# Kernel optimization log

Measured on AMD Instinct MI355X. Metric: run time of the kernel, lower is better.

## Reference

```python
import jax, jax.numpy as jnp
import numpy as np
from jax import lax

# Static config (matches init_kwargs)
D_MODEL = 1024
EXPAND = 2
D_INNER = D_MODEL * EXPAND          # 2048
HEAD_DIM = 64
N_HEADS = D_INNER // HEAD_DIM       # 32
N_GROUPS = 1
D_STATE = 128
D_CONV = 4
CONV_DIM = D_INNER + 2 * N_GROUPS * D_STATE        # 2304
D_IN_PROJ = 2 * D_INNER + 2 * N_GROUPS * D_STATE + N_HEADS  # 4384
SEQLEN = 8192
LN_EPS = 1e-5


def setup_inputs() -> dict:
    key = jax.random.key(0)
    ks = jax.random.split(key, 6)
    x = jax.random.normal(ks[0], (SEQLEN, D_MODEL), jnp.float32)
    W_in = jax.random.normal(ks[1], (D_IN_PROJ, D_MODEL), jnp.float32) / np.sqrt(D_MODEL)
    W_conv = jax.random.normal(ks[2], (CONV_DIM, 1, D_CONV), jnp.float32) / np.sqrt(D_CONV)
    b_conv = jnp.zeros((CONV_DIM,), jnp.float32)
    # dt_bias init per Mamba2: dt ~ LogUniform(dt_min, dt_max), inverse-softplus
    dt = jnp.exp(jax.random.uniform(ks[3], (N_HEADS,)) * (np.log(0.1) - np.log(0.001)) + np.log(0.001))
    dt = jnp.clip(dt, 1e-4)
    dt_bias = dt + jnp.log(-jnp.expm1(-dt))
    A_log = jnp.log(jax.random.uniform(ks[4], (N_HEADS,), minval=1.0, maxval=16.0))
    D_param = jnp.ones((N_HEADS,), jnp.float32)
    ln_w = jnp.ones((D_INNER,), jnp.float32)
    ln_b = jnp.zeros((D_INNER,), jnp.float32)
    W_out = jax.random.normal(ks[5], (D_MODEL, D_INNER), jnp.float32) / np.sqrt(D_INNER)
    return dict(x=x, W_in=W_in, W_conv=W_conv, b_conv=b_conv, dt_bias=dt_bias,
                A_log=A_log, D_param=D_param, ln_w=ln_w, ln_b=ln_b, W_out=W_out)


def reference(x, W_in, W_conv, b_conv, dt_bias, A_log, D_param, ln_w, ln_b, W_out):
    L = x.shape[0]
    zxbcdt = x @ W_in.T                                   # (L, d_in_proj)
    z = zxbcdt[:, :D_INNER]                               # gate
    xbc = zxbcdt[:, D_INNER:D_INNER + CONV_DIM]           # (L, conv_dim)
    dt = jax.nn.softplus(zxbcdt[:, D_INNER + CONV_DIM:] + dt_bias)  # (L, h)
    # depthwise causal-window conv with SAME padding over the sequence
    lhs = xbc.T[None]                                      # (1, conv_dim, L)
    conv = lax.conv_general_dilated(lhs, W_conv, (1,), 'SAME',
                                    feature_group_count=CONV_DIM,
                                    dimension_numbers=('NCH', 'OIH', 'NCH'))[0]
    xbc = jax.nn.silu((conv + b_conv[:, None]).T)          # (L, conv_dim)
    x_ssm = xbc[:, :D_INNER].reshape(L, N_HEADS, HEAD_DIM)
    B = xbc[:, D_INNER:D_INNER + N_GROUPS * D_STATE].reshape(L, N_GROUPS, D_STATE)
    C = xbc[:, D_INNER + N_GROUPS * D_STATE:].reshape(L, N_GROUPS, D_STATE)
    hpg = N_HEADS // N_GROUPS
    Bh = jnp.repeat(B, hpg, axis=1)                        # (L, h, n)
    Ch = jnp.repeat(C, hpg, axis=1)                        # (L, h, n)
    A = -jnp.exp(A_log)                                    # (h,), negative
    a = jnp.exp(dt * A)                                    # (L, h) per-token decay in (0,1)
    V = x_ssm * dt[..., None]                              # discretized input (L, h, p)
    # non-causal SSD (VSSD): global state H then readout, plus D skip
    H = jnp.einsum('lhn,lh,lhp->hnp', Bh, a, V)            # (h, n, p)
    y = jnp.einsum('lhn,hnp->lhp', Ch, H) + D_param[None, :, None] * x_ssm
    y = y.reshape(L, D_INNER)
    # LayerNorm (eqx default: weight+bias, eps=1e-5), then gate by z
    mu = jnp.mean(y, axis=-1, keepdims=True)
    var = jnp.var(y, axis=-1, keepdims=True)
    y = ((y - mu) / jnp.sqrt(var + LN_EPS)) * ln_w + ln_b
    y = y * z
    return y @ W_out.T                                     # (L, d_model)
```

## Files before the change

kernel.cpp:

```cpp
#include <hip/hip_runtime.h>
#include <hip/hip_bf16.h>
#include <math.h>

#define L_SEQ 8192
#define DM 1024
#define DI 2048
#define NH 32
#define HD 64
#define DS 128
#define CDIM 2304
#define DPROJ 4384
#define NPAD_IN 4608
#define KSPLIT 8
#define OPROWS 2176

typedef short bf16x8 __attribute__((ext_vector_type(8)));
typedef float floatx4 __attribute__((ext_vector_type(4)));
typedef unsigned short u16x4 __attribute__((ext_vector_type(4)));
typedef unsigned short u16x8 __attribute__((ext_vector_type(8)));

#define AS1(p) ((const __attribute__((address_space(1))) void*)(p))
#define AS3(p) ((__attribute__((address_space(3))) void*)(p))

__device__ __forceinline__ float bf2f(unsigned short u) {
  union { unsigned int i; float f; } c; c.i = ((unsigned int)u) << 16; return c.f;
}
__device__ __forceinline__ unsigned short f2bf(float f) {
  return __bfloat16_as_ushort(__float2bfloat16(f));
}

__global__ __launch_bounds__(512, 2)
void gemm256_8ph(const unsigned short* __restrict__ A, int lda,
                 const unsigned short* __restrict__ B, int ldb,
                 unsigned short* __restrict__ C, int ldc,
                 int K, int Nstore) {
  __shared__ __align__(16) char lds[131072];
  const int t = threadIdx.x;
  const int lane = t & 63;
  const int w = t >> 6;
  const int wm = w & 1, wn = w >> 1;
  const int fr = lane & 15, quad = lane >> 4;

  int gx = gridDim.x, gy = gridDim.y;
  int linear = blockIdx.y * gx + blockIdx.x;
  int xcd = linear & 7, loc = linear >> 3;
  int mper = gy >> 3;
  int mt = xcd * mper + loc % mper;
  int nt = loc / mper;
  const int m0 = mt << 8, n0 = nt << 8;
  const int NT = K >> 6;

  floatx4 acc[8][4];
#pragma unroll
  for (int i = 0; i < 8; ++i)
#pragma unroll
    for (int j = 0; j < 4; ++j) acc[i][j] = (floatx4){0.f, 0.f, 0.f, 0.f};
  bf16x8 af[4][2], b0[2][2], b1[2][2];

  auto stA = [&](int buf, int kt, int g) {
#pragma unroll
    for (int i = 0; i < 2; ++i) {
      int o = (i * 512 + t) * 16;
      int os = o ^ (((o >> 7) & 7) << 4);
      int rloc = os >> 7, kb = os & 127;
      int R = ((rloc >> 6) << 7) | (g << 6) | (rloc & 63);
      const unsigned short* src = A + (size_t)(m0 + R) * lda + (kt << 6) + (kb >> 1);
      __builtin_amdgcn_global_load_lds(AS1(src),
          AS3(lds + buf * 32768 + g * 16384 + o), 16, 0, 0);
    }
  };
  auto stB = [&](int buf, int kt, int g) {
#pragma unroll
    for (int i = 0; i < 2; ++i) {
      int o = (i * 512 + t) * 16;
      int os = o ^ (((o >> 7) & 7) << 4);
      int rloc = os >> 7, kb = os & 127;
      int R = ((rloc >> 5) << 6) | (g << 5) | (rloc & 31);
      const unsigned short* src = B + (size_t)(n0 + R) * ldb + (kt << 6) + (kb >> 1);
      __builtin_amdgcn_global_load_lds(AS1(src),
          AS3(lds + 65536 + buf * 32768 + g * 16384 + o), 16, 0, 0);
    }
  };
  auto rdA = [&](int buf, int mi, int ks) -> bf16x8 {
    int rloc = (wm << 6) | ((mi & 3) << 4) | fr;
    return *(const bf16x8*)(lds + buf * 32768 + (mi >> 2) * 16384 + rloc * 128 +
                            (((ks << 6) | (quad << 4)) ^ ((fr & 7) << 4)));
  };
  auto rdB = [&](int buf, int ni, int ks) -> bf16x8 {
    int rloc = (wn << 5) | ((ni & 1) << 4) | fr;
    return *(const bf16x8*)(lds + 65536 + buf * 32768 + (ni >> 1) * 16384 + rloc * 128 +
                            (((ks << 6) | (quad << 4)) ^ ((fr & 7) << 4)));
  };

  stA(0, 0, 0); stB(0, 0, 0); stB(0, 0, 1); stA(0, 0, 1);
  if (NT > 1) { stA(1, 1, 0); stB(1, 1, 0); stB(1, 1, 1); }
  if (NT > 1) asm volatile("s_waitcnt vmcnt(6)" ::: "memory");
  else        asm volatile("s_waitcnt vmcnt(0)" ::: "memory");
  __builtin_amdgcn_s_barrier();

  for (int kt = 0; kt < NT; ++kt) {
    const int buf = kt & 1;
    const bool pf1 = (kt + 1 < NT);
    const bool pf2 = (kt + 2 < NT);
#pragma unroll
    for (int mi = 0; mi < 4; ++mi) { af[mi][0] = rdA(buf, mi, 0); af[mi][1] = rdA(buf, mi, 1); }
#pragma unroll
    for (int ni = 0; ni < 2; ++ni) { b0[ni][0] = rdB(buf, ni, 0); b0[ni][1] = rdB(buf, ni, 1); }
    if (pf1) stA(buf ^ 1, kt + 1, 1);
    asm volatile("s_waitcnt lgkmcnt(8)" ::: "memory");
    __builtin_amdgcn_s_barrier();
    asm volatile("s_waitcnt lgkmcnt(0)" ::: "memory");
    __builtin_amdgcn_s_setprio(1);
#pragma unroll
    for (int mi = 0; mi < 4; ++mi)
#pragma unroll
      for (int ni = 0; ni < 2; ++ni)
#pragma unroll
        for (int ks = 0; ks < 2; ++ks)
          acc[mi][ni] = __builtin_amdgcn_mfma_f32_16x16x32_bf16(af[mi][ks], b0[ni][ks], acc[mi][ni], 0, 0, 0);
    __builtin_amdgcn_s_setprio(0);
    __builtin_amdgcn_s_barrier();
#pragma unroll
    for (int ni = 0; ni < 2; ++ni) { b1[ni][0] = rdB(buf, ni + 2, 0); b1[ni][1] = rdB(buf, ni + 2, 1); }
    if (pf2) stA(buf, kt + 2, 0);
    __builtin_amdgcn_s_barrier();
    asm volatile("s_waitcnt lgkmcnt(0)" ::: "memory");
    __builtin_amdgcn_s_setprio(1);
#pragma unroll
    for (int mi = 0; mi < 4; ++mi)
#pragma unroll
      for (int ni = 0; ni < 2; ++ni)
#pragma unroll
        for (int ks = 0; ks < 2; ++ks)
          acc[mi][ni + 2] = __builtin_amdgcn_mfma_f32_16x16x32_bf16(af[mi][ks], b1[ni][ks], acc[mi][ni + 2], 0, 0, 0);
    __builtin_amdgcn_s_setprio(0);
    __builtin_amdgcn_s_barrier();
#pragma unroll
    for (int mi = 0; mi < 4; ++mi) { af[mi][0] = rdA(buf, mi + 4, 0); af[mi][1] = rdA(buf, mi + 4, 1); }
    if (pf2) stB(buf, kt + 2, 0);
    __builtin_amdgcn_s_barrier();
    asm volatile("s_waitcnt lgkmcnt(0)" ::: "memory");
    __builtin_amdgcn_s_setprio(1);
#pragma unroll
    for (int mi = 0; mi < 4; ++mi)
#pragma unroll
      for (int ni = 0; ni < 2; ++ni)
#pragma unroll
        for (int ks = 0; ks < 2; ++ks)
          acc[mi + 4][ni + 2] = __builtin_amdgcn_mfma_f32_16x16x32_bf16(af[mi][ks], b1[ni][ks], acc[mi + 4][ni + 2], 0, 0, 0);
    __builtin_amdgcn_s_setprio(0);
    __builtin_amdgcn_s_barrier();
    if (pf2) stB(buf, kt + 2, 1);
    __builtin_amdgcn_s_barrier();
    __builtin_amdgcn_s_setprio(1);
#pragma unroll
    for (int mi = 0; mi < 4; ++mi)
#pragma unroll
      for (int ni = 0; ni < 2; ++ni)
#pragma unroll
        for (int ks = 0; ks < 2; ++ks)
          acc[mi + 4][ni] = __builtin_amdgcn_mfma_f32_16x16x32_bf16(af[mi][ks], b0[ni][ks], acc[mi + 4][ni], 0, 0, 0);
    __builtin_amdgcn_s_setprio(0);
    if (kt < NT - 1) {
      if (pf2) asm volatile("s_waitcnt vmcnt(6)" ::: "memory");
      else     asm volatile("s_waitcnt vmcnt(0)" ::: "memory");
      __builtin_amdgcn_s_barrier();
    }
  }

  unsigned short* rp = (unsigned short*)lds;
  const int mb = wm * 128, nb = wn * 64;
#pragma unroll
  for (int mi = 0; mi < 8; ++mi)
#pragma unroll
    for (int ni = 0; ni < 4; ++ni)
#pragma unroll
      for (int r = 0; r < 4; ++r)
        rp[(mb + mi * 16 + quad * 4 + r) * 256 + nb + ni * 16 + fr] = f2bf(acc[mi][ni][r]);
  __syncthreads();
#pragma unroll
  for (int j = 0; j < 16; ++j) {
    int lin = j * 4096 + t * 8;
    int row = lin >> 8, col = lin & 255;
    int gcol = n0 + col;
    if (gcol < Nstore)
      *(u16x8*)&C[(size_t)(m0 + row) * ldc + gcol] = *(const u16x8*)&rp[lin];
  }
}

template <int MODE>
__global__ __launch_bounds__(256)
void gemm_bt_mfma(const unsigned short* __restrict__ A, int lda,
                  const unsigned short* __restrict__ B, int ldb,
                  void* __restrict__ Cout, int ldc,
                  int Kfull, int Nstore,
                  const unsigned short* __restrict__ xs,
                  const float* __restrict__ Dvec) {
  __shared__ __align__(16) char smem[17408];
  unsigned short* Asm = (unsigned short*)smem;
  unsigned short* Bsm = Asm + 128 * 32;
  const int t = threadIdx.x;

  int bx = blockIdx.x, by = blockIdx.y;
  if (MODE != 2) {
    int gx = gridDim.x;
    int linear = by * gx + bx;
    int xcd = linear & 7;
    int local = linear >> 3;
    by = xcd * 8 + (local & 7);
    bx = local >> 3;
  }
  const int m0 = by * 128;
  const int n0 = bx * 128;

  int kstart = 0, klen = Kfull;
  if (MODE == 2) { klen = Kfull / KSPLIT; kstart = blockIdx.z * klen; }
  const int wave = t >> 6, lane = t & 63;
  const int wm = (wave & 1) * 64;
  const int wn = (wave >> 1) * 64;
  const int fr = lane & 15;
  const int quad = lane >> 4;

  floatx4 acc[4][4];
#pragma unroll
  for (int i = 0; i < 4; ++i)
#pragma unroll
    for (int j = 0; j < 4; ++j) acc[i][j] = (floatx4){0.f, 0.f, 0.f, 0.f};

  for (int k0 = kstart; k0 < kstart + klen; k0 += 32) {
#pragma unroll
    for (int i = 0; i < 2; ++i) {
      int linear = i * 256 + t;
      int row = linear >> 2;
      int kq = (linear & 3) * 8;
      const unsigned short* ga = A + (size_t)(m0 + row) * lda + (k0 + kq);
      const unsigned short* gb = B + (size_t)(n0 + row) * ldb + (k0 + kq);
      __builtin_amdgcn_global_load_lds(AS1(ga), AS3(&Asm[linear * 8]), 16, 0, 0);
      __builtin_amdgcn_global_load_lds(AS1(gb), AS3(&Bsm[linear * 8]), 16, 0, 0);
    }
    __syncthreads();

    bf16x8 af[4], bfr[4];
#pragma unroll
    for (int i = 0; i < 4; ++i) {
      af[i]  = *(const bf16x8*)&Asm[(wm + i * 16 + fr) * 32 + quad * 8];
      bfr[i] = *(const bf16x8*)&Bsm[(wn + i * 16 + fr) * 32 + quad * 8];
    }
#pragma unroll
    for (int mi = 0; mi < 4; ++mi)
#pragma unroll
      for (int ni = 0; ni < 4; ++ni)
        acc[mi][ni] = __builtin_amdgcn_mfma_f32_16x16x32_bf16(
            af[mi], bfr[ni], acc[mi][ni], 0, 0, 0);
    __syncthreads();
  }

  const int lrbase = (wm ? 16 : 0) + quad * 4;
  if (MODE == 0 || MODE == 1) {
    unsigned short(*rp)[136] = (unsigned short(*)[136])smem;
    unsigned short* C = (unsigned short*)Cout;
#pragma unroll
    for (int mi = 0; mi < 4; ++mi) {
      __syncthreads();
#pragma unroll
      for (int ni = 0; ni < 4; ++ni)
#pragma unroll
        for (int r = 0; r < 4; ++r)
          rp[lrbase + r][wn + ni * 16 + fr] = f2bf(acc[mi][ni][r]);
      __syncthreads();
#pragma unroll
      for (int j = 0; j < 2; ++j) {
        int off = j * 2048 + t * 8;
        int lr = off >> 7, c = off & 127;
        int grow = m0 + (lr >> 4) * 64 + mi * 16 + (lr & 15);
        int gcol = n0 + c;
        u16x8 v = *(const u16x8*)&rp[lr][c];
        if (MODE == 1) {
          u16x8 xv = *(const u16x8*)&xs[(size_t)grow * ldc + gcol];
          float Dh = Dvec[gcol >> 6];
          u16x8 o;
#pragma unroll
          for (int e = 0; e < 8; ++e) o[e] = f2bf(bf2f(v[e]) + Dh * bf2f(xv[e]));
          *(u16x8*)&C[(size_t)grow * ldc + gcol] = o;
        } else {
          if (gcol < Nstore) *(u16x8*)&C[(size_t)grow * ldc + gcol] = v;
        }
      }
    }
  } else {
    float(*rpf)[136] = (float(*)[136])smem;
    float* C = (float*)Cout;
    if (MODE == 2) C += (size_t)blockIdx.z * DS * DI;
#pragma unroll
    for (int mi = 0; mi < 4; ++mi) {
      __syncthreads();
#pragma unroll
      for (int ni = 0; ni < 4; ++ni)
#pragma unroll
        for (int r = 0; r < 4; ++r)
          rpf[lrbase + r][wn + ni * 16 + fr] = acc[mi][ni][r];
      __syncthreads();
#pragma unroll
      for (int j = 0; j < 4; ++j) {
        int off = j * 1024 + t * 4;
        int lr = off >> 7, c = off & 127;
        int grow = m0 + (lr >> 4) * 64 + mi * 16 + (lr & 15);
        int gcol = n0 + c;
        float4 v = *(const float4*)&rpf[lr][c];
        *(float4*)&C[(size_t)grow * ldc + gcol] = v;
      }
    }
  }
}

__global__ __launch_bounds__(256)
void cast_all_kernel(const float* __restrict__ x, const float* __restrict__ W_in,
                     const float* __restrict__ W_out,
                     unsigned short* __restrict__ x_bf16,
                     unsigned short* __restrict__ win_bf16,
                     unsigned short* __restrict__ wout_bf16) {
  int b = blockIdx.x;
  int t = threadIdx.x;
  u16x4 o = (u16x4){0, 0, 0, 0};
  if (b < 8192) {
    size_t i4 = ((size_t)b * 256 + t) * 4;
    float4 v = *(const float4*)(x + i4);
    o.x = f2bf(v.x); o.y = f2bf(v.y); o.z = f2bf(v.z); o.w = f2bf(v.w);
    *(u16x4*)(x_bf16 + i4) = o;
  } else if (b < 12800) {
    size_t i4 = ((size_t)(b - 8192) * 256 + t) * 4;
    int row = (int)(i4 >> 10);
    if (row < DPROJ) {
      float4 v = *(const float4*)(W_in + i4);
      o.x = f2bf(v.x); o.y = f2bf(v.y); o.z = f2bf(v.z); o.w = f2bf(v.w);
    }
    *(u16x4*)(win_bf16 + i4) = o;
  } else {
    size_t i4 = ((size_t)(b - 12800) * 256 + t) * 4;
    float4 v = *(const float4*)(W_out + i4);
    o.x = f2bf(v.x); o.y = f2bf(v.y); o.z = f2bf(v.z); o.w = f2bf(v.w);
    *(u16x4*)(wout_bf16 + i4) = o;
  }
}

__global__ __launch_bounds__(256)
void dt_kernel(const unsigned short* __restrict__ zxb, const float* __restrict__ dt_bias,
               const float* __restrict__ A_log, float* __restrict__ s_out) {
  int idx = blockIdx.x * 256 + threadIdx.x;
  int l = idx >> 5, h = idx & 31;
  float v = bf2f(zxb[(size_t)l * DPROJ + (DI + CDIM) + h]) + dt_bias[h];
  float d = (v > 20.f) ? v : log1pf(expf(v));
  s_out[idx] = d * expf(-d * expf(A_log[h]));
}

__global__ __launch_bounds__(256)
void conv_fused_kernel(const unsigned short* __restrict__ zxb,
                       const float* __restrict__ Wc,
                       const float* __restrict__ bc,
                       const float* __restrict__ svec,
                       unsigned short* __restrict__ xs,
                       unsigned short* __restrict__ cb,
                       unsigned short* __restrict__ OpT) {
  __shared__ unsigned short zt[67][66];
  __shared__ unsigned short ot[64][66];
  __shared__ float sl[64];
  const int c0 = blockIdx.x * 64;
  const int l0 = blockIdx.y * 64;
  const int t = threadIdx.x;
  for (int idx = t; idx < 67 * 16; idx += 256) {
    int row = idx >> 4;
    int colq = (idx & 15) * 4;
    int gl = l0 - 1 + row;
    u16x4 v = (u16x4){0, 0, 0, 0};
    if (gl >= 0 && gl < L_SEQ)
      v = *(const u16x4*)&zxb[(size_t)gl * DPROJ + DI + c0 + colq];
    *(u16x4*)&zt[row][colq] = v;
  }
  const bool isX = (c0 < DI);
  const bool isC = (c0 >= DI + DS);
  if (isX && t < 64) sl[t] = svec[(size_t)(l0 + t) * NH + (c0 >> 6)];
  const int c = t & 63;
  const int gc = c0 + c;
  const float4 wv = *(const float4*)&Wc[gc * 4];
  const float bias = bc[gc];
  const int lq = (t >> 6) * 16;
  __syncthreads();
#pragma unroll
  for (int i = 0; i < 16; ++i) {
    int ll = lq + i;
    float sacc = bias + bf2f(zt[ll][c]) * wv.x + bf2f(zt[ll + 1][c]) * wv.y +
                 bf2f(zt[ll + 2][c]) * wv.z + bf2f(zt[ll + 3][c]) * wv.w;
    float v = sacc / (1.f + expf(-sacc));
    int gl = l0 + ll;
    if (isC) {
      cb[(size_t)gl * DS + (gc - (DI + DS))] = f2bf(v);
    } else if (isX) {
      xs[(size_t)gl * DI + gc] = f2bf(v);
      ot[c][ll] = f2bf(v * sl[ll]);
    } else {
      ot[c][ll] = f2bf(v);
    }
  }
  if (!isC) {
    __syncthreads();
#pragma unroll
    for (int j = 0; j < 4; ++j) {
      int linear = j * 1024 + t * 4;
      int rr = linear >> 6;
      int lc = linear & 63;
      *(u16x4*)&OpT[(size_t)(c0 + rr) * L_SEQ + l0 + lc] = *(const u16x4*)&ot[rr][lc];
    }
  }
}

__global__ __launch_bounds__(256)
void h_reduce_t_kernel(const float* __restrict__ P, unsigned short* __restrict__ Ht) {
  __shared__ float tile[32][65];
  const int bid = blockIdx.x;
  const int pt = bid & 31, ng = bid >> 5;
  const int t = threadIdx.x;
#pragma unroll
  for (int i = 0; i < 8; ++i) {
    int nl = i * 4 + (t >> 6);
    int n = ng * 32 + nl;
    int p = pt * 64 + (t & 63);
    float acc = 0.f;
#pragma unroll
    for (int z = 0; z < KSPLIT; ++z)
      acc += P[(size_t)z * (DS * DI) + (size_t)n * DI + p];
    tile[nl][t & 63] = acc;
  }
  __syncthreads();
#pragma unroll
  for (int j = 0; j < 8; ++j) {
    int linear = j * 256 + t;
    int pl = linear >> 5, nl = linear & 31;
    Ht[(size_t)(pt * 64 + pl) * DS + ng * 32 + nl] = f2bf(tile[nl][pl]);
  }
}

__global__ __launch_bounds__(256)
void ln_mul_kernel(const unsigned short* __restrict__ ybuf, unsigned short* __restrict__ zxb,
                   const float* __restrict__ ln_w, const float* __restrict__ ln_b) {
  int l = blockIdx.x;
  int t = threadIdx.x;
  int c0 = t * 8;
  u16x8 yv = *(const u16x8*)&ybuf[(size_t)l * DI + c0];
  float vals[8];
  float s = 0.f, sq = 0.f;
#pragma unroll
  for (int i = 0; i < 8; ++i) {
    float v = bf2f(yv[i]);
    vals[i] = v;
    s += v;
    sq += v * v;
  }
#pragma unroll
  for (int off = 32; off > 0; off >>= 1) {
    s += __shfl_down(s, off, 64);
    sq += __shfl_down(sq, off, 64);
  }
  __shared__ float red[10];
  int wave = t >> 6, lane = t & 63;
  if (lane == 0) { red[wave] = s; red[4 + wave] = sq; }
  __syncthreads();
  if (t == 0) {
    float S = red[0] + red[1] + red[2] + red[3];
    float SQ = red[4] + red[5] + red[6] + red[7];
    float mu = S / (float)DI;
    red[8] = mu;
    red[9] = rsqrtf(SQ / (float)DI - mu * mu + 1e-5f);
  }
  __syncthreads();
  float mu = red[8], rstd = red[9];
  unsigned short* zrow = zxb + (size_t)l * DPROJ;
  u16x8 zv = *(const u16x8*)&zrow[c0];
  float4 w0 = *(const float4*)&ln_w[c0], w1 = *(const float4*)&ln_w[c0 + 4];
  float4 b0 = *(const float4*)&ln_b[c0], b1 = *(const float4*)&ln_b[c0 + 4];
  float w[8] = {w0.x, w0.y, w0.z, w0.w, w1.x, w1.y, w1.z, w1.w};
  float b[8] = {b0.x, b0.y, b0.z, b0.w, b1.x, b1.y, b1.z, b1.w};
  u16x8 o;
#pragma unroll
  for (int i = 0; i < 8; ++i) {
    float v = (vals[i] - mu) * rstd * w[i] + b[i];
    o[i] = f2bf(v * bf2f(zv[i]));
  }
  *(u16x8*)&zrow[DI + c0] = o;
}

extern "C" void kernel_launch(void* const* d_in, const int* in_sizes, int n_in,
                              void* d_out, int out_size, void* d_ws, size_t ws_size,
                              hipStream_t stream) {
  const float* x       = (const float*)d_in[0];
  const float* W_in    = (const float*)d_in[1];
  const float* W_conv  = (const float*)d_in[2];
  const float* b_conv  = (const float*)d_in[3];
  const float* dt_bias = (const float*)d_in[4];
  const float* A_log   = (const float*)d_in[5];
  const float* D_param = (const float*)d_in[6];
  const float* ln_w    = (const float*)d_in[7];
  const float* ln_b    = (const float*)d_in[8];
  const float* W_out   = (const float*)d_in[9];
  float* out = (float*)d_out;

  unsigned short* zxb = (unsigned short*)d_ws;
  unsigned short* xs   = zxb + (size_t)L_SEQ * DPROJ;
  unsigned short* cb   = xs + (size_t)L_SEQ * DI;
  float* svec = (float*)(cb + (size_t)L_SEQ * DS);
  unsigned short* OpT = (unsigned short*)(svec + (size_t)L_SEQ * NH);
  float* Ppart = (float*)(OpT + (size_t)OPROWS * L_SEQ);
  unsigned short* Ht = (unsigned short*)(Ppart + (size_t)KSPLIT * DS * DI);
  unsigned short* wout_bf16 = Ht + (size_t)DI * DS;
  unsigned short* x_bf16   = OpT;
  unsigned short* win_bf16 = OpT + (size_t)L_SEQ * DM;
  unsigned short* ybuf     = OpT;

  cast_all_kernel<<<14848, 256, 0, stream>>>(x, W_in, W_out, x_bf16, win_bf16,
                                             wout_bf16);

  gemm256_8ph<<<dim3(NPAD_IN / 256, L_SEQ / 256), 512, 0, stream>>>(
      x_bf16, DM, win_bf16, DM, zxb, DPROJ, DM, DPROJ);

  dt_kernel<<<(L_SEQ * NH) / 256, 256, 0, stream>>>(zxb, dt_bias, A_log, svec);

  conv_fused_kernel<<<dim3(CDIM / 64, L_SEQ / 64), 256, 0, stream>>>(
      zxb, W_conv, b_conv, svec, xs, cb, OpT);

  gemm_bt_mfma<2><<<dim3(DI / 128, 1, KSPLIT), 256, 0, stream>>>(
      OpT + (size_t)DI * L_SEQ, L_SEQ, OpT, L_SEQ, Ppart, DI, L_SEQ, DI,
      nullptr, nullptr);

  h_reduce_t_kernel<<<128, 256, 0, stream>>>(Ppart, Ht);

  gemm_bt_mfma<1><<<dim3(DI / 128, L_SEQ / 128), 256, 0, stream>>>(
      cb, DS, Ht, DS, ybuf, DI, DS, DI, xs, D_param);

  ln_mul_kernel<<<L_SEQ, 256, 0, stream>>>(ybuf, zxb, ln_w, ln_b);

  gemm_bt_mfma<3><<<dim3(DM / 128, L_SEQ / 128), 256, 0, stream>>>(
      zxb + DI, DPROJ, wout_bf16, DI, out, DM, DI, DM, nullptr, nullptr);
}
```

Baseline: 369.5 us.

## Shrink input-proj GEMM tile to 128x256 and reuse it for output projection

Turns the 256x256 8-phase input-projection GEMM into a templated 128x256 variant with a reworked pipeline, so more blocks are launched. The output projection moves from the smaller 128x128 MFMA kernel to this kernel, with a direct fp32 store epilogue. The H-state GEMM split-K factor also doubles, giving more parallelism but more partial sums to reduce. Smaller tiles cost more global traffic per flop, and the changed vmcnt waits are a correctness risk.

```diff
diff --git a/kernel.cpp b/kernel.cpp
--- a/kernel.cpp
+++ b/kernel.cpp
@@ -11,7 +11,7 @@
 #define CDIM 2304
 #define DPROJ 4384
 #define NPAD_IN 4608
-#define KSPLIT 8
+#define KSPLIT 16
 #define OPROWS 2176
 
 typedef short bf16x8 __attribute__((ext_vector_type(8)));
@@ -29,12 +29,13 @@
   return __bfloat16_as_ushort(__float2bfloat16(f));
 }
 
+template <int OMODE>
 __global__ __launch_bounds__(512, 2)
-void gemm256_8ph(const unsigned short* __restrict__ A, int lda,
+void gemm128_8ph(const unsigned short* __restrict__ A, int lda,
                  const unsigned short* __restrict__ B, int ldb,
-                 unsigned short* __restrict__ C, int ldc,
+                 void* __restrict__ Cout, int ldc,
                  int K, int Nstore) {
-  __shared__ __align__(16) char lds[131072];
+  __shared__ __align__(16) char lds[98304];
   const int t = threadIdx.x;
   const int lane = t & 63;
   const int w = t >> 6;
@@ -47,26 +48,24 @@
   int mper = gy >> 3;
   int mt = xcd * mper + loc % mper;
   int nt = loc / mper;
-  const int m0 = mt << 8, n0 = nt << 8;
+  const int m0 = mt << 7, n0 = nt << 8;
   const int NT = K >> 6;
 
-  floatx4 acc[8][4];
-#pragma unroll
-  for (int i = 0; i < 8; ++i)
+  floatx4 acc[4][4];
+#pragma unroll
+  for (int i = 0; i < 4; ++i)
 #pragma unroll
     for (int j = 0; j < 4; ++j) acc[i][j] = (floatx4){0.f, 0.f, 0.f, 0.f};
   bf16x8 af[4][2], b0[2][2], b1[2][2];
 
-  auto stA = [&](int buf, int kt, int g) {
+  auto stA = [&](int buf, int kt) {
 #pragma unroll
     for (int i = 0; i < 2; ++i) {
       int o = (i * 512 + t) * 16;
       int os = o ^ (((o >> 7) & 7) << 4);
       int rloc = os >> 7, kb = os & 127;
-      int R = ((rloc >> 6) << 7) | (g << 6) | (rloc & 63);
-      const unsigned short* src = A + (size_t)(m0 + R) * lda + (kt << 6) + (kb >> 1);
-      __builtin_amdgcn_global_load_lds(AS1(src),
-          AS3(lds + buf * 32768 + g * 16384 + o), 16, 0, 0);
+      const unsigned short* src = A + (size_t)(m0 + rloc) * lda + (kt << 6) + (kb >> 1);
+      __builtin_amdgcn_global_load_lds(AS1(src), AS3(lds + buf * 16384 + o), 16, 0, 0);
     }
   };
   auto stB = [&](int buf, int kt, int g) {
@@ -78,24 +77,27 @@
       int R = ((rloc >> 5) << 6) | (g << 5) | (rloc & 31);
       const unsigned short* src = B + (size_t)(n0 + R) * ldb + (kt << 6) + (kb >> 1);
       __builtin_amdgcn_global_load_lds(AS1(src),
-          AS3(lds + 65536 + buf * 32768 + g * 16384 + o), 16, 0, 0);
+          AS3(lds + 32768 + buf * 32768 + g * 16384 + o), 16, 0, 0);
     }
   };
   auto rdA = [&](int buf, int mi, int ks) -> bf16x8 {
-    int rloc = (wm << 6) | ((mi & 3) << 4) | fr;
-    return *(const bf16x8*)(lds + buf * 32768 + (mi >> 2) * 16384 + rloc * 128 +
+    int rloc = (wm << 6) | (mi << 4) | fr;
+    return *(const bf16x8*)(lds + buf * 16384 + rloc * 128 +
                             (((ks << 6) | (quad << 4)) ^ ((fr & 7) << 4)));
   };
   auto rdB = [&](int buf, int ni, int ks) -> bf16x8 {
     int rloc = (wn << 5) | ((ni & 1) << 4) | fr;
-    return *(const bf16x8*)(lds + 65536 + buf * 32768 + (ni >> 1) * 16384 + rloc * 128 +
+    return *(const bf16x8*)(lds + 32768 + buf * 32768 + (ni >> 1) * 16384 + rloc * 128 +
                             (((ks << 6) | (quad << 4)) ^ ((fr & 7) << 4)));
   };
 
-  stA(0, 0, 0); stB(0, 0, 0); stB(0, 0, 1); stA(0, 0, 1);
-  if (NT > 1) { stA(1, 1, 0); stB(1, 1, 0); stB(1, 1, 1); }
-  if (NT > 1) asm volatile("s_waitcnt vmcnt(6)" ::: "memory");
-  else        asm volatile("s_waitcnt vmcnt(0)" ::: "memory");
+  stA(0, 0); stB(0, 0, 0); stB(0, 0, 1);
+  if (NT > 1) {
+    stA(1, 1); stB(1, 1, 0);
+    asm volatile("s_waitcnt vmcnt(4)" ::: "memory");
+  } else {
+    asm volatile("s_waitcnt vmcnt(0)" ::: "memory");
+  }
   __builtin_amdgcn_s_barrier();
 
   for (int kt = 0; kt < NT; ++kt) {
@@ -106,7 +108,7 @@
     for (int mi = 0; mi < 4; ++mi) { af[mi][0] = rdA(buf, mi, 0); af[mi][1] = rdA(buf, mi, 1); }
 #pragma unroll
     for (int ni = 0; ni < 2; ++ni) { b0[ni][0] = rdB(buf, ni, 0); b0[ni][1] = rdB(buf, ni, 1); }
-    if (pf1) stA(buf ^ 1, kt + 1, 1);
+    if (pf1) stB(buf ^ 1, kt + 1, 1);
     asm volatile("s_waitcnt lgkmcnt(8)" ::: "memory");
     __builtin_amdgcn_s_barrier();
     asm volatile("s_waitcnt lgkmcnt(0)" ::: "memory");
@@ -119,10 +121,11 @@
         for (int ks = 0; ks < 2; ++ks)
           acc[mi][ni] = __builtin_amdgcn_mfma_f32_16x16x32_bf16(af[mi][ks], b0[ni][ks], acc[mi][ni], 0, 0, 0);
     __builtin_amdgcn_s_setprio(0);
+    asm volatile("s_waitcnt vmcnt(6)" ::: "memory");
     __builtin_amdgcn_s_barrier();
 #pragma unroll
     for (int ni = 0; ni < 2; ++ni) { b1[ni][0] = rdB(buf, ni + 2, 0); b1[ni][1] = rdB(buf, ni + 2, 1); }
-    if (pf2) stA(buf, kt + 2, 0);
+    if (pf2) { stA(buf, kt + 2); stB(buf, kt + 2, 0); }
     __builtin_amdgcn_s_barrier();
     asm volatile("s_waitcnt lgkmcnt(0)" ::: "memory");
     __builtin_amdgcn_s_setprio(1);
@@ -133,33 +136,6 @@
 #pragma unroll
         for (int ks = 0; ks < 2; ++ks)
           acc[mi][ni + 2] = __builtin_amdgcn_mfma_f32_16x16x32_bf16(af[mi][ks], b1[ni][ks], acc[mi][ni + 2], 0, 0, 0);
-    __builtin_amdgcn_s_setprio(0);
-    __builtin_amdgcn_s_barrier();
-#pragma unroll
-    for (int mi = 0; mi < 4; ++mi) { af[mi][0] = rdA(buf, mi + 4, 0); af[mi][1] = rdA(buf, mi + 4, 1); }
-    if (pf2) stB(buf, kt + 2, 0);
-    __builtin_amdgcn_s_barrier();
-    asm volatile("s_waitcnt lgkmcnt(0)" ::: "memory");
-    __builtin_amdgcn_s_setprio(1);
-#pragma unroll
-    for (int mi = 0; mi < 4; ++mi)
-#pragma unroll
-      for (int ni = 0; ni < 2; ++ni)
-#pragma unroll
-        for (int ks = 0; ks < 2; ++ks)
-          acc[mi + 4][ni + 2] = __builtin_amdgcn_mfma_f32_16x16x32_bf16(af[mi][ks], b1[ni][ks], acc[mi + 4][ni + 2], 0, 0, 0);
-    __builtin_amdgcn_s_setprio(0);
-    __builtin_amdgcn_s_barrier();
-    if (pf2) stB(buf, kt + 2, 1);
-    __builtin_amdgcn_s_barrier();
-    __builtin_amdgcn_s_setprio(1);
-#pragma unroll
-    for (int mi = 0; mi < 4; ++mi)
-#pragma unroll
-      for (int ni = 0; ni < 2; ++ni)
-#pragma unroll
-        for (int ks = 0; ks < 2; ++ks)
-          acc[mi + 4][ni] = __builtin_amdgcn_mfma_f32_16x16x32_bf16(af[mi][ks], b0[ni][ks], acc[mi + 4][ni], 0, 0, 0);
     __builtin_amdgcn_s_setprio(0);
     if (kt < NT - 1) {
       if (pf2) asm volatile("s_waitcnt vmcnt(6)" ::: "memory");
@@ -168,23 +144,39 @@
     }
   }
 
-  unsigned short* rp = (unsigned short*)lds;
-  const int mb = wm * 128, nb = wn * 64;
-#pragma unroll
-  for (int mi = 0; mi < 8; ++mi)
-#pragma unroll
-    for (int ni = 0; ni < 4; ++ni)
-#pragma unroll
-      for (int r = 0; r < 4; ++r)
-        rp[(mb + mi * 16 + quad * 4 + r) * 256 + nb + ni * 16 + fr] = f2bf(acc[mi][ni][r]);
-  __syncthreads();
-#pragma unroll
-  for (int j = 0; j < 16; ++j) {
-    int lin = j * 4096 + t * 8;
-    int row = lin >> 8, col = lin & 255;
-    int gcol = n0 + col;
-    if (gcol < Nstore)
-      *(u16x8*)&C[(size_t)(m0 + row) * ldc + gcol] = *(const u16x8*)&rp[lin];
+  if (OMODE == 0) {
+    unsigned short* rp = (unsigned short*)lds;
+    unsigned short* C = (unsigned short*)Cout;
+    const int mb = wm * 64, nb = wn * 64;
+#pragma unroll
+    for (int mi = 0; mi < 4; ++mi)
+#pragma unroll
+      for (int ni = 0; ni < 4; ++ni)
+#pragma unroll
+        for (int r = 0; r < 4; ++r)
+          rp[(mb + mi * 16 + quad * 4 + r) * 256 + nb + ni * 16 + fr] = f2bf(acc[mi][ni][r]);
+    __syncthreads();
+#pragma unroll
+    for (int j = 0; j < 8; ++j) {
+      int lin = j * 4096 + t * 8;
+      int row = lin >> 8, col = lin & 255;
+      int gcol = n0 + col;
+      if (gcol < Nstore)
+        *(u16x8*)&C[(size_t)(m0 + row) * ldc + gcol] = *(const u16x8*)&rp[lin];
+    }
+  } else {
+    float* Cf = (float*)Cout;
+#pragma unroll
+    for (int mi = 0; mi < 4; ++mi)
+#pragma unroll
+      for (int ni = 0; ni < 4; ++ni) {
+        int gcol = n0 + wn * 64 + ni * 16 + fr;
+        int grow = m0 + wm * 64 + mi * 16 + quad * 4;
+#pragma unroll
+        for (int r = 0; r < 4; ++r)
+          if (gcol < Nstore)
+            Cf[(size_t)(grow + r) * ldc + gcol] = acc[mi][ni][r];
+      }
   }
 }
 
@@ -518,7 +510,7 @@
   cast_all_kernel<<<14848, 256, 0, stream>>>(x, W_in, W_out, x_bf16, win_bf16,
                                              wout_bf16);
 
-  gemm256_8ph<<<dim3(NPAD_IN / 256, L_SEQ / 256), 512, 0, stream>>>(
+  gemm128_8ph<0><<<dim3(NPAD_IN / 256, L_SEQ / 128), 512, 0, stream>>>(
       x_bf16, DM, win_bf16, DM, zxb, DPROJ, DM, DPROJ);
 
   dt_kernel<<<(L_SEQ * NH) / 256, 256, 0, stream>>>(zxb, dt_bias, A_log, svec);
@@ -537,6 +529,6 @@
 
   ln_mul_kernel<<<L_SEQ, 256, 0, stream>>>(ybuf, zxb, ln_w, ln_b);
 
-  gemm_bt_mfma<3><<<dim3(DM / 128, L_SEQ / 128), 256, 0, stream>>>(
-      zxb + DI, DPROJ, wout_bf16, DI, out, DM, DI, DM, nullptr, nullptr);
-}
+  gemm128_8ph<1><<<dim3(DM / 256, L_SEQ / 128), 512, 0, stream>>>(
+      zxb + DI, DPROJ, wout_bf16, DI, out, DM, DI, DM);
+}
```

Result: faster. 340.2 us (-7.9%).
